# Performance work log

Measured on AMD Instinct MI355X. Metric: run time of the kernel, lower is better.

The kernel has to match this reference:

```python
import jax, jax.numpy as jnp
import numpy as np

D_MODEL = 512
D_STATE = 16
D_CONV = 4
EXPAND = 2
HEADDIM = 64
D_INNER = EXPAND * D_MODEL            # 1024
NHEADS = D_INNER // HEADDIM           # 16
CONV_DIM = D_INNER + 2 * D_STATE      # 1056 (x, B, C channels)
D_IN_PROJ = 2 * D_INNER + 2 * D_STATE + NHEADS  # 2096
EPS = 1e-5
B_SZ, L_SEQ = 8, 4096


def _mamba_param_keys(prefix):
    return [prefix + n for n in
            ('in_proj', 'conv_w', 'conv_b', 'dt_bias', 'A_log', 'D', 'norm_w', 'out_proj')]


def _make_mamba_params(key, prefix):
    ks = jax.random.split(key, 4)
    s = 0.02
    return {
        prefix + 'in_proj': jax.random.normal(ks[0], (D_IN_PROJ, D_MODEL), jnp.float32) * s,
        prefix + 'conv_w': jax.random.normal(ks[1], (CONV_DIM, D_CONV), jnp.float32) * s,
        prefix + 'conv_b': jnp.zeros((CONV_DIM,), jnp.float32),
        prefix + 'dt_bias': jax.random.normal(ks[2], (NHEADS,), jnp.float32) * 0.1,
        prefix + 'A_log': jnp.log(jnp.arange(1, NHEADS + 1, dtype=jnp.float32)),
        prefix + 'D': jnp.ones((NHEADS,), jnp.float32),
        prefix + 'norm_w': jnp.ones((D_INNER,), jnp.float32),
        prefix + 'out_proj': jax.random.normal(ks[3], (D_MODEL, D_INNER), jnp.float32) * s,
    }


def setup_inputs() -> dict:
    key = jax.random.key(0)
    kx, kf, kb, kp = jax.random.split(key, 4)
    inp = {'x': jax.random.normal(kx, (B_SZ, L_SEQ, D_MODEL), jnp.float32)}
    inp.update(_make_mamba_params(kf, 'f_'))
    inp.update(_make_mamba_params(kb, 'b_'))
    kp1, kp2 = jax.random.split(kp)
    inp['proj_w'] = jax.random.normal(kp1, (D_MODEL, 2 * D_MODEL), jnp.float32) * 0.02
    inp['proj_b'] = jnp.zeros((D_MODEL,), jnp.float32)
    inp['ln_w'] = jnp.ones((D_MODEL,), jnp.float32)
    inp['ln_b'] = jnp.zeros((D_MODEL,), jnp.float32)
    return inp


def mamba2(x, in_proj, conv_w, conv_b, dt_bias, A_log, Dp, norm_w, out_proj):
    """Mamba2 block (ngroups=1): in_proj -> causal depthwise conv -> selective scan -> gated RMSNorm -> out_proj."""
    B, L, _ = x.shape
    zxbcdt = x @ in_proj.T                               # [B,L,2096]
    z = zxbcdt[..., :D_INNER]                            # gate
    xBC = zxbcdt[..., D_INNER:D_INNER + CONV_DIM]
    dt = jax.nn.softplus(zxbcdt[..., D_INNER + CONV_DIM:] + dt_bias)  # [B,L,H]
    # causal depthwise conv over (x, B, C) channels + SiLU
    xp = jnp.pad(xBC, ((0, 0), (D_CONV - 1, 0), (0, 0)))
    conv = conv_b + sum(xp[:, k:k + L, :] * conv_w[:, k] for k in range(D_CONV))
    xBC = jax.nn.silu(conv)
    xs = xBC[..., :D_INNER].reshape(B, L, NHEADS, HEADDIM)  # [B,L,H,P]
    Bm = xBC[..., D_INNER:D_INNER + D_STATE]                # [B,L,N]
    Cm = xBC[..., D_INNER + D_STATE:]                       # [B,L,N]
    A = -jnp.exp(A_log)                                     # [H]
    dA = jnp.exp(dt * A)                                    # [B,L,H]

    def step(h, inp):
        dA_t, dt_t, x_t, B_t, C_t = inp                     # [B,H],[B,H],[B,H,P],[B,N],[B,N]
        h = h * dA_t[..., None, None] + (dt_t[..., None] * x_t)[..., None] * B_t[:, None, None, :]
        y = jnp.einsum('bhpn,bn->bhp', h, C_t)
        return h, y

    h0 = jnp.zeros((B, NHEADS, HEADDIM, D_STATE), x.dtype)
    inps = (dA.transpose(1, 0, 2), dt.transpose(1, 0, 2), xs.transpose(1, 0, 2, 3),
            Bm.transpose(1, 0, 2), Cm.transpose(1, 0, 2))
    _, ys = jax.lax.scan(step, h0, inps)                    # ys: [L,B,H,P]
    y = ys.transpose(1, 0, 2, 3) + Dp[:, None] * xs         # skip connection
    y = y.reshape(B, L, D_INNER)
    # gated RMSNorm (norm_before_gate=False)
    y = y * jax.nn.silu(z)
    y = y * jax.lax.rsqrt(jnp.mean(y * y, axis=-1, keepdims=True) + EPS) * norm_w
    return y @ out_proj.T


def _layer_norm(x, w, b):
    mu = jnp.mean(x, axis=-1, keepdims=True)
    v = jnp.var(x, axis=-1, keepdims=True)
    return (x - mu) * jax.lax.rsqrt(v + EPS) * w + b


def reference(x,
              f_in_proj, f_conv_w, f_conv_b, f_dt_bias, f_A_log, f_D, f_norm_w, f_out_proj,
              b_in_proj, b_conv_w, b_conv_b, b_dt_bias, b_A_log, b_D, b_norm_w, b_out_proj,
              proj_w, proj_b, ln_w, ln_b):
    x_fwd = mamba2(x, f_in_proj, f_conv_w, f_conv_b, f_dt_bias, f_A_log, f_D, f_norm_w, f_out_proj)
    x_bwd = jnp.flip(
        mamba2(jnp.flip(x, axis=1), b_in_proj, b_conv_w, b_conv_b, b_dt_bias, b_A_log, b_D, b_norm_w, b_out_proj),
        axis=1)
    comb = jnp.concatenate([x_fwd, x_bwd], axis=-1)         # [B,L,2D]
    out = comb @ proj_w.T + proj_b                          # dropout is identity (eval / p=0)
    return _layer_norm(x + out, ln_w, ln_b)
```

## Files before the change

### kernel.cpp

```cpp
#include <hip/hip_runtime.h>
#include <hip/hip_bf16.h>
#include <math.h>

typedef __bf16 bf16x8_t __attribute__((ext_vector_type(8)));
typedef float f32x4_t __attribute__((ext_vector_type(4)));
typedef unsigned short u16x8_t __attribute__((ext_vector_type(8)));
typedef unsigned short u16x4_t __attribute__((ext_vector_type(4)));

#define DEV __device__ __forceinline__

DEV float bf2f(unsigned short u) {
    unsigned int v = ((unsigned int)u) << 16;
    return __builtin_bit_cast(float, v);
}
DEV unsigned short f2bf(float f) {
    unsigned int u = __builtin_bit_cast(unsigned int, f);
    u += 0x7fffu + ((u >> 16) & 1u);
    return (unsigned short)(u >> 16);
}

__global__ __launch_bounds__(256) void cvt_k(
    const float* __restrict__ in, unsigned short* __restrict__ out, int n8)
{
    int t = blockIdx.x * 256 + threadIdx.x;
    if (t >= n8) return;
    f32x4_t a = ((const f32x4_t*)in)[t * 2];
    f32x4_t b = ((const f32x4_t*)in)[t * 2 + 1];
    u16x8_t o;
#pragma unroll
    for (int j = 0; j < 4; j++) { o[j] = f2bf(a[j]); o[4 + j] = f2bf(b[j]); }
    ((u16x8_t*)out)[t] = o;
}

template <int NT, bool FLIP_A, bool FLIP_C, bool OUT_F32, bool ADD_BIAS, bool ACCUM>
__global__ __launch_bounds__(256, 2) void gemm_bt(
    const unsigned short* __restrict__ A,
    const unsigned short* __restrict__ W,
    void* __restrict__ Cout,
    const float* __restrict__ bias,
    int N, int K, int ldc, int col_ofs)
{
    __shared__ __attribute__((aligned(16))) unsigned char smem[49152];
    const int tid  = threadIdx.x;
    const int wave = tid >> 6;
    const int lane = tid & 63;

    int mtile_i, ntile_i;
    if (NT == 0) {
        mtile_i = blockIdx.y;
        ntile_i = blockIdx.x;
    } else {
        const int L = blockIdx.x;
        const int MTl = (int)gridDim.x / NT;
        const int ppx = MTl >> 3;
        const int xcd = L & 7, q = L >> 3;
        mtile_i = xcd * ppx + q / NT;
        ntile_i = q % NT;
    }
    const int mtile = mtile_i << 7;
    const int ntile = ntile_i << 7;

    const int c0 = tid, c1 = 256 + tid;
    const int r0 = c0 >> 2, p0 = c0 & 3, g0 = p0 ^ ((r0 >> 1) & 3);
    const int r1 = c1 >> 2, p1 = c1 & 3, g1 = p1 ^ ((r1 >> 1) & 3);

    int am0 = mtile + r0; if (FLIP_A) am0 ^= 4095;
    int am1 = mtile + r1; if (FLIP_A) am1 ^= 4095;
    const unsigned short* aP0 = A + (size_t)am0 * K + g0 * 8;
    const unsigned short* aP1 = A + (size_t)am1 * K + g1 * 8;

    int wr0 = ntile + r0; if (wr0 > N - 1) wr0 = N - 1;
    int wr1 = ntile + r1; if (wr1 > N - 1) wr1 = N - 1;
    const unsigned short* wP0 = W + (size_t)wr0 * K + g0 * 8;
    const unsigned short* wP1 = W + (size_t)wr1 * K + g1 * 8;

    const int stago = wave * 1024;

    f32x4_t acc[4][4] = {};

    const int wm = (wave & 1) << 6;
    const int wn = (wave >> 1) << 6;
    const int r    = lane & 15;
    const int quad = lane >> 4;
    const int sw   = (r >> 1) & 3;

    int aoff[4], woff[4];
#pragma unroll
    for (int i = 0; i < 4; i++) {
        int m = wm + i * 16 + r;
        aoff[i] = (m * 4 + (quad ^ sw)) * 16;
        int n = wn + i * 16 + r;
        woff[i] = (n * 4 + (quad ^ sw)) * 16 + 8192;
    }

    auto STAGE = [&](int kt, int bufsel) {
        const int k0 = kt << 5;
        unsigned char* base = smem + bufsel * 16384;
        __builtin_amdgcn_global_load_lds(
            (const __attribute__((address_space(1))) void*)(aP0 + k0),
            (__attribute__((address_space(3))) void*)(base + stago), 16, 0, 0);
        __builtin_amdgcn_global_load_lds(
            (const __attribute__((address_space(1))) void*)(aP1 + k0),
            (__attribute__((address_space(3))) void*)(base + 4096 + stago), 16, 0, 0);
        __builtin_amdgcn_global_load_lds(
            (const __attribute__((address_space(1))) void*)(wP0 + k0),
            (__attribute__((address_space(3))) void*)(base + 8192 + stago), 16, 0, 0);
        __builtin_amdgcn_global_load_lds(
            (const __attribute__((address_space(1))) void*)(wP1 + k0),
            (__attribute__((address_space(3))) void*)(base + 12288 + stago), 16, 0, 0);
    };

    const int nt = K >> 5;
    STAGE(0, 0);
    if (nt > 1) STAGE(1, 1);

    for (int kt = 0; kt < nt; kt++) {
        if (kt + 1 < nt) asm volatile("s_waitcnt vmcnt(4)" ::: "memory");
        else             asm volatile("s_waitcnt vmcnt(0)" ::: "memory");
        __builtin_amdgcn_s_barrier();
        __builtin_amdgcn_sched_barrier(0);

        if (kt + 2 < nt) STAGE(kt + 2, (kt + 2) % 3);

        const unsigned char* bufc = smem + (kt % 3) * 16384;
        bf16x8_t af[4], wf[4];
#pragma unroll
        for (int i = 0; i < 4; i++)
            af[i] = __builtin_bit_cast(bf16x8_t, *(const u16x8_t*)(bufc + aoff[i]));
#pragma unroll
        for (int j = 0; j < 4; j++)
            wf[j] = __builtin_bit_cast(bf16x8_t, *(const u16x8_t*)(bufc + woff[j]));
#pragma unroll
        for (int i = 0; i < 4; i++)
#pragma unroll
            for (int j = 0; j < 4; j++)
                acc[i][j] = __builtin_amdgcn_mfma_f32_16x16x32_bf16(af[i], wf[j], acc[i][j], 0, 0, 0);
        __builtin_amdgcn_sched_barrier(0);
        __builtin_amdgcn_s_barrier();
    }

#pragma unroll
    for (int i = 0; i < 4; i++) {
#pragma unroll
        for (int j = 0; j < 4; j++) {
            int cc = ntile + wn + j * 16 + r;
            if (cc >= N) continue;
#pragma unroll
            for (int reg = 0; reg < 4; reg++) {
                int rr = mtile + wm + i * 16 + quad * 4 + reg;
                int orow = FLIP_C ? (rr ^ 4095) : rr;
                float v = acc[i][j][reg];
                if (ADD_BIAS) v += bias[cc];
                if (OUT_F32) {
                    float* p = (float*)Cout + (size_t)orow * ldc + col_ofs + cc;
                    if (ACCUM) v += *p;
                    *p = v;
                } else {
                    ((unsigned short*)Cout)[(size_t)orow * ldc + col_ofs + cc] = f2bf(v);
                }
            }
        }
    }
}

__global__ __launch_bounds__(256) void pack_pw_k(
    const float* __restrict__ pw, unsigned short* __restrict__ pwb)
{
    int t = blockIdx.x * 256 + threadIdx.x;
    int j8 = t & 63;
    int n  = (t >> 6) & 511;
    int dir = t >> 15;
    const float* src = pw + (size_t)n * 1024 + dir * 512 + j8 * 8;
    f32x4_t a = *(const f32x4_t*)src;
    f32x4_t b = *(const f32x4_t*)(src + 4);
    u16x8_t o;
#pragma unroll
    for (int j = 0; j < 4; j++) { o[j] = f2bf(a[j]); o[4 + j] = f2bf(b[j]); }
    *(u16x8_t*)(pwb + (size_t)dir * 512 * 512 + (size_t)n * 512 + j8 * 8) = o;
}

__global__ __launch_bounds__(256) void tr_op_k(
    const float* __restrict__ op0, const float* __restrict__ op1,
    unsigned short* __restrict__ opT)
{
    __shared__ float tile[32][33];
    const int dir = blockIdx.z;
    const float* op = dir ? op1 : op0;
    const int k0 = blockIdx.x * 32;
    const int j0 = blockIdx.y * 32;
    const int tx = threadIdx.x & 31, ty = threadIdx.x >> 5;
#pragma unroll
    for (int i = 0; i < 4; i++) {
        int j = j0 + ty + i * 8;
        tile[ty + i * 8][tx] = op[(size_t)j * 1024 + k0 + tx];
    }
    __syncthreads();
    unsigned short* dst = opT + (size_t)dir * 1024 * 512;
#pragma unroll
    for (int i = 0; i < 4; i++) {
        int k = k0 + ty + i * 8;
        dst[(size_t)k * 512 + j0 + tx] = f2bf(tile[tx][ty + i * 8]);
    }
}

__global__ __launch_bounds__(256) void conv_silu_k(
    const unsigned short* __restrict__ xin,
    const float* __restrict__ cw,
    const float* __restrict__ cb,
    unsigned short* __restrict__ outp)
{
    int t = blockIdx.x * 256 + threadIdx.x;
    int c8 = t % 132;
    int rb = t / 132;
    int c = c8 * 8;
    int row0 = rb * 8;
    int l0 = row0 & 4095;

    float w[8][4];
#pragma unroll
    for (int j = 0; j < 8; j++) {
        f32x4_t wv = *(const f32x4_t*)(cw + (c + j) * 4);
        w[j][0] = wv[0]; w[j][1] = wv[1]; w[j][2] = wv[2]; w[j][3] = wv[3];
    }
    float bia[8];
    {
        f32x4_t b0 = *(const f32x4_t*)(cb + c);
        f32x4_t b1 = *(const f32x4_t*)(cb + c + 4);
#pragma unroll
        for (int j = 0; j < 4; j++) { bia[j] = b0[j]; bia[4 + j] = b1[j]; }
    }

    u16x8_t zero;
#pragma unroll
    for (int j = 0; j < 8; j++) zero[j] = 0;

    u16x8_t win[11];
#pragma unroll
    for (int u = 0; u < 11; u++) {
        int lu = l0 - 3 + u;
        win[u] = (lu >= 0)
            ? *(const u16x8_t*)(xin + (size_t)(row0 - 3 + u) * 1072 + c)
            : zero;
    }

#pragma unroll
    for (int s = 0; s < 8; s++) {
        float acc[8];
#pragma unroll
        for (int j = 0; j < 8; j++) acc[j] = bia[j];
#pragma unroll
        for (int k = 0; k < 4; k++) {
            u16x8_t xv = win[s + k];
#pragma unroll
            for (int j = 0; j < 8; j++)
                acc[j] = fmaf(bf2f(xv[j]), w[j][k], acc[j]);
        }
        u16x8_t o;
#pragma unroll
        for (int j = 0; j < 8; j++) {
            float xx = acc[j];
            o[j] = f2bf(xx * __builtin_amdgcn_rcpf(1.f + __expf(-xx)));
        }
        *(u16x8_t*)(outp + (size_t)(row0 + s) * 1056 + c) = o;
    }
}

__global__ __launch_bounds__(256) void dt_pre_k(
    const unsigned short* __restrict__ xin,
    const float* __restrict__ dt_bias,
    const float* __restrict__ A_log,
    float* __restrict__ dtb, float* __restrict__ ldab)
{
    int t = blockIdx.x * 256 + threadIdx.x;
    int h = t & 15;
    int row = t >> 4;
    float x = bf2f(xin[(size_t)row * 1072 + 1056 + h]) + dt_bias[h];
    float dt = (x > 20.f) ? x : log1pf(__expf(x));
    float A = -__expf(A_log[h]);
    dtb[t] = dt;
    ldab[t] = dt * A;
}

DEV void stage_xt(const unsigned short* __restrict__ xrow, unsigned short* XtW, int l)
{
    u16x8_t xv[8];
#pragma unroll
    for (int m = 0; m < 8; m++) xv[m] = *(const u16x8_t*)(xrow + m * 8);
#pragma unroll
    for (int p = 0; p < 64; p++) {
        int blkc = (l >> 3) ^ (p & 7);
        XtW[p * 64 + blkc * 8 + (l & 7)] = xv[p >> 3][p & 7];
    }
}

DEV bf16x8_t xt_frag(const unsigned short* XtW, int r, int quad, int jj, int kk)
{
    int p = jj * 16 + r;
    int blkc = (kk * 4 + quad) ^ (p & 7);
    return __builtin_bit_cast(bf16x8_t, *(const u16x8_t*)(XtW + p * 64 + blkc * 8));
}

__global__ __launch_bounds__(256) void scan_chstate_k(
    const unsigned short* __restrict__ xc,
    const float* __restrict__ dtb,
    float* __restrict__ lcs,
    float* __restrict__ Hend, float* __restrict__ dec)
{
    __shared__ __attribute__((aligned(16))) unsigned char sm[37120];
    unsigned short* Btr = (unsigned short*)sm;
    float* csW = (float*)(sm + 2304);
    float* dtW = (float*)(sm + 3328);
    unsigned short* Xt0 = (unsigned short*)(sm + 4352);

    const int tid = threadIdx.x;
    const int w = tid >> 6, l = tid & 63;
    const int r = l & 15, quad = l >> 4;
    const int row0 = blockIdx.x * 64;
    const int b = blockIdx.x >> 6, chunk = blockIdx.x & 63;
    const int h = blockIdx.y * 4 + w;
    const int blk = ((b * 16 + h) << 6) | chunk;

    {
        int n = tid & 15, s0 = (tid >> 4) * 4;
#pragma unroll
        for (int js = 0; js < 4; js++) {
            int s = s0 + js;
            Btr[n * 72 + s] = xc[(size_t)(row0 + s) * 1056 + 1024 + n];
        }
    }

    float v   = lcs[(size_t)(row0 + l) * 16 + h];
    float dtv = dtb[(size_t)(row0 + l) * 16 + h];
#pragma unroll
    for (int d = 1; d < 64; d <<= 1) {
        float o = __shfl_up(v, d, 64);
        if (l >= d) v += o;
    }
    lcs[(size_t)(row0 + l) * 16 + h] = v;
    csW[w * 64 + l] = v;
    dtW[w * 64 + l] = dtv;
    if (l == 63) dec[blk] = __expf(v);
    __syncthreads();

    unsigned short* XtW = Xt0 + w * 4096;
    stage_xt(xc + (size_t)(row0 + l) * 1056 + h * 64, XtW, l);

    const float* csr = csW + w * 64;
    const float* dtr = dtW + w * 64;
    float cs63 = csr[63];

    f32x4_t z = {0.f, 0.f, 0.f, 0.f};
    f32x4_t hacc[4] = {z, z, z, z};
#pragma unroll
    for (int kk = 0; kk < 2; kk++) {
        int sb = kk * 32 + quad * 8;
        u16x8_t bv = *(const u16x8_t*)(Btr + r * 72 + sb);
        f32x4_t c0 = *(const f32x4_t*)(csr + sb);
        f32x4_t c1 = *(const f32x4_t*)(csr + sb + 4);
        f32x4_t d0 = *(const f32x4_t*)(dtr + sb);
        f32x4_t d1 = *(const f32x4_t*)(dtr + sb + 4);
        u16x8_t wv;
#pragma unroll
        for (int j = 0; j < 4; j++) {
            wv[j]     = f2bf(bf2f(bv[j])     * d0[j] * __expf(cs63 - c0[j]));
            wv[4 + j] = f2bf(bf2f(bv[4 + j]) * d1[j] * __expf(cs63 - c1[j]));
        }
        bf16x8_t wf = __builtin_bit_cast(bf16x8_t, wv);
#pragma unroll
        for (int jj = 0; jj < 4; jj++)
            hacc[jj] = __builtin_amdgcn_mfma_f32_16x16x32_bf16(wf, xt_frag(XtW, r, quad, jj, kk), hacc[jj], 0, 0, 0);
    }
    float* o = Hend + (size_t)blk * 1024;
#pragma unroll
    for (int jj = 0; jj < 4; jj++)
#pragma unroll
        for (int reg = 0; reg < 4; reg++)
            o[(jj * 16 + r) * 16 + quad * 4 + reg] = hacc[jj][reg];
}

__global__ __launch_bounds__(64) void scan_comb_k(float* __restrict__ H, const float* __restrict__ dec)
{
    int bh = blockIdx.x >> 2;
    int q  = blockIdx.x & 3;
    int t  = threadIdx.x;
    float* base = H + (size_t)bh * 64 * 1024 + q * 256 + t * 4;
    const float* dp = dec + bh * 64;
    f32x4_t hs = {0.f, 0.f, 0.f, 0.f};
    f32x4_t cur = *(const f32x4_t*)base;
    for (int c = 0; c < 64; c++) {
        int cn = (c < 63) ? c + 1 : 63;
        f32x4_t nxt = *(const f32x4_t*)(base + (size_t)cn * 1024);
        float d = dp[c];
        *(f32x4_t*)(base + (size_t)c * 1024) = hs;
#pragma unroll
        for (int j = 0; j < 4; j++) hs[j] = fmaf(hs[j], d, cur[j]);
        cur = nxt;
    }
}

__global__ __launch_bounds__(256) void scan_chout_k(
    const unsigned short* __restrict__ xc,
    const float* __restrict__ dtb, const float* __restrict__ csb,
    const float* __restrict__ Hst, const float* __restrict__ Dp,
    unsigned short* __restrict__ ybuf)
{
    __shared__ __attribute__((aligned(16))) unsigned char sm[60416];
    unsigned short* Ct = (unsigned short*)sm;
    unsigned short* Bt = (unsigned short*)(sm + 4096);
    float* S   = (float*)(sm + 8192);
    float* csL = (float*)(sm + 25600);
    float* dtL = (float*)(sm + 26624);
    unsigned short* Xt0 = (unsigned short*)(sm + 27648);

    const int tid = threadIdx.x;
    const int w = tid >> 6, l = tid & 63;
    const int r = l & 15, quad = l >> 4;
    const int row0 = blockIdx.x * 64;
    const int b = blockIdx.x >> 6, chunk = blockIdx.x & 63;
    const int h = blockIdx.y * 4 + w;
    const int blk = ((b * 16 + h) << 6) | chunk;

    {
        int rowi = tid >> 2, seg = tid & 3;
        u16x8_t vb, vc;
        if (seg < 2) {
            const unsigned short* src = xc + (size_t)(row0 + rowi) * 1056 + 1024 + seg * 8;
            vb = *(const u16x8_t*)src;
            vc = *(const u16x8_t*)(src + 16);
        } else {
#pragma unroll
            for (int j = 0; j < 8; j++) { vb[j] = 0; vc[j] = 0; }
        }
        *(u16x8_t*)(Bt + rowi * 32 + seg * 8) = vb;
        *(u16x8_t*)(Ct + rowi * 32 + seg * 8) = vc;
    }
    csL[w * 64 + l] = csb[(size_t)(row0 + l) * 16 + h];
    dtL[w * 64 + l] = dtb[(size_t)(row0 + l) * 16 + h];
    __syncthreads();

    {
        bf16x8_t cf = __builtin_bit_cast(bf16x8_t, *(const u16x8_t*)(Ct + (w * 16 + r) * 32 + quad * 8));
        f32x4_t z = {0.f, 0.f, 0.f, 0.f};
#pragma unroll
        for (int j = 0; j < 4; j++) {
            bf16x8_t bfv = __builtin_bit_cast(bf16x8_t, *(const u16x8_t*)(Bt + (j * 16 + r) * 32 + quad * 8));
            f32x4_t d = __builtin_amdgcn_mfma_f32_16x16x32_bf16(cf, bfv, z, 0, 0, 0);
#pragma unroll
            for (int reg = 0; reg < 4; reg++)
                S[(w * 16 + quad * 4 + reg) * 68 + j * 16 + r] = d[reg];
        }
    }
    __syncthreads();

    unsigned short* XtW = Xt0 + w * 4096;
    stage_xt(xc + (size_t)(row0 + l) * 1056 + h * 64, XtW, l);

    const float* csr = csL + w * 64;
    const float* dtr = dtL + w * 64;

    f32x4_t acc[4][4];
    {
        bf16x8_t hf[4];
#pragma unroll
        for (int jj = 0; jj < 4; jj++) {
            int p = jj * 16 + r;
            u16x8_t hv;
            if (quad < 2) {
                const float* hp = Hst + (size_t)blk * 1024 + p * 16 + quad * 8;
                f32x4_t h0 = *(const f32x4_t*)hp;
                f32x4_t h1 = *(const f32x4_t*)(hp + 4);
#pragma unroll
                for (int j = 0; j < 4; j++) { hv[j] = f2bf(h0[j]); hv[4 + j] = f2bf(h1[j]); }
            } else {
#pragma unroll
                for (int j = 0; j < 8; j++) hv[j] = 0;
            }
            hf[jj] = __builtin_bit_cast(bf16x8_t, hv);
        }
        f32x4_t z = {0.f, 0.f, 0.f, 0.f};
#pragma unroll
        for (int i = 0; i < 4; i++) {
            bf16x8_t cf = __builtin_bit_cast(bf16x8_t, *(const u16x8_t*)(Ct + (i * 16 + r) * 32 + quad * 8));
#pragma unroll
            for (int jj = 0; jj < 4; jj++)
                acc[i][jj] = __builtin_amdgcn_mfma_f32_16x16x32_bf16(cf, hf[jj], z, 0, 0, 0);
        }
#pragma unroll
        for (int i = 0; i < 4; i++) {
            f32x4_t es;
#pragma unroll
            for (int reg = 0; reg < 4; reg++) es[reg] = __expf(csr[i * 16 + quad * 4 + reg]);
#pragma unroll
            for (int jj = 0; jj < 4; jj++)
#pragma unroll
                for (int reg = 0; reg < 4; reg++) acc[i][jj][reg] *= es[reg];
        }
    }

#pragma unroll
    for (int kk = 0; kk < 2; kk++) {
        int sb = kk * 32 + quad * 8;
        bf16x8_t xf[4];
#pragma unroll
        for (int jj = 0; jj < 4; jj++) xf[jj] = xt_frag(XtW, r, quad, jj, kk);
        f32x4_t c0 = *(const f32x4_t*)(csr + sb);
        f32x4_t c1 = *(const f32x4_t*)(csr + sb + 4);
        f32x4_t d0 = *(const f32x4_t*)(dtr + sb);
        f32x4_t d1 = *(const f32x4_t*)(dtr + sb + 4);
#pragma unroll
        for (int i = 0; i < 4; i++) {
            int t = i * 16 + r;
            float cst = csr[t];
            const float* Srow = S + t * 68;
            f32x4_t s0 = *(const f32x4_t*)(Srow + sb);
            f32x4_t s1 = *(const f32x4_t*)(Srow + sb + 4);
            u16x8_t wv;
#pragma unroll
            for (int j = 0; j < 4; j++) {
                int s = sb + j;
                float v0 = (s <= t) ? __expf(cst - c0[j]) * d0[j] * s0[j] : 0.f;
                wv[j] = f2bf(v0);
                int s2 = sb + 4 + j;
                float v1 = (s2 <= t) ? __expf(cst - c1[j]) * d1[j] * s1[j] : 0.f;
                wv[4 + j] = f2bf(v1);
            }
            bf16x8_t wf = __builtin_bit_cast(bf16x8_t, wv);
#pragma unroll
            for (int jj = 0; jj < 4; jj++)
                acc[i][jj] = __builtin_amdgcn_mfma_f32_16x16x32_bf16(wf, xf[jj], acc[i][jj], 0, 0, 0);
        }
    }

    float Dh = Dp[h];
#pragma unroll
    for (int i = 0; i < 4; i++) {
#pragma unroll
        for (int jj = 0; jj < 4; jj++) {
            int p = jj * 16 + r;
            int t0 = i * 16 + quad * 4;
            int blk2 = (t0 >> 3) ^ (p & 7);
            u16x4_t x4 = *(const u16x4_t*)(XtW + p * 64 + blk2 * 8 + (t0 & 7));
#pragma unroll
            for (int reg = 0; reg < 4; reg++) {
                float yv = fmaf(Dh, bf2f(x4[reg]), acc[i][jj][reg]);
                ybuf[(size_t)(row0 + t0 + reg) * 1024 + h * 64 + p] = f2bf(yv);
            }
        }
    }
}

__global__ __launch_bounds__(256) void rmsgate_k(
    unsigned short* __restrict__ y,
    const unsigned short* __restrict__ z,
    const float* __restrict__ nw)
{
    const int wave = threadIdx.x >> 6, lane = threadIdx.x & 63;
    const size_t row = (size_t)blockIdx.x * 4 + wave;
    const int c = lane * 16;
    unsigned short* yp = y + row * 1024 + c;
    const unsigned short* zp = z + row * 1024 + c;
    u16x8_t yv0 = *(const u16x8_t*)yp;
    u16x8_t yv1 = *(const u16x8_t*)(yp + 8);
    u16x8_t zv0 = *(const u16x8_t*)zp;
    u16x8_t zv1 = *(const u16x8_t*)(zp + 8);
    float g[16];
    float ss = 0.f;
#pragma unroll
    for (int j = 0; j < 8; j++) {
        float zf = bf2f(zv0[j]);
        float sil = zf * __builtin_amdgcn_rcpf(1.f + __expf(-zf));
        g[j] = bf2f(yv0[j]) * sil;
        ss += g[j] * g[j];
    }
#pragma unroll
    for (int j = 0; j < 8; j++) {
        float zf = bf2f(zv1[j]);
        float sil = zf * __builtin_amdgcn_rcpf(1.f + __expf(-zf));
        g[8 + j] = bf2f(yv1[j]) * sil;
        ss += g[8 + j] * g[8 + j];
    }
#pragma unroll
    for (int m = 32; m > 0; m >>= 1) ss += __shfl_xor(ss, m, 64);
    float scale = rsqrtf(ss * (1.f / 1024.f) + 1e-5f);
    f32x4_t w0 = *(const f32x4_t*)(nw + c);
    f32x4_t w1 = *(const f32x4_t*)(nw + c + 4);
    f32x4_t w2 = *(const f32x4_t*)(nw + c + 8);
    f32x4_t w3 = *(const f32x4_t*)(nw + c + 12);
    u16x8_t o0, o1;
#pragma unroll
    for (int j = 0; j < 4; j++) {
        o0[j]     = f2bf(g[j]      * scale * w0[j]);
        o0[4 + j] = f2bf(g[4 + j]  * scale * w1[j]);
        o1[j]     = f2bf(g[8 + j]  * scale * w2[j]);
        o1[4 + j] = f2bf(g[12 + j] * scale * w3[j]);
    }
    *(u16x8_t*)yp = o0;
    *(u16x8_t*)(yp + 8) = o1;
}

__global__ __launch_bounds__(256) void ln_k(
    const float* __restrict__ x,
    const float* __restrict__ f,
    const float* __restrict__ lw,
    const float* __restrict__ lb,
    float* __restrict__ outp)
{
    const int wave = threadIdx.x >> 6, lane = threadIdx.x & 63;
    const size_t row = (size_t)blockIdx.x * 4 + wave;
    const int c = lane * 8;
    f32x4_t xv0 = *(const f32x4_t*)(x + row * 512 + c);
    f32x4_t xv1 = *(const f32x4_t*)(x + row * 512 + c + 4);
    f32x4_t fv0 = *(const f32x4_t*)(f + row * 512 + c);
    f32x4_t fv1 = *(const f32x4_t*)(f + row * 512 + c + 4);
    float s[8];
    float sum = 0.f, sq = 0.f;
#pragma unroll
    for (int j = 0; j < 4; j++) {
        s[j] = xv0[j] + fv0[j];
        s[4 + j] = xv1[j] + fv1[j];
    }
#pragma unroll
    for (int j = 0; j < 8; j++) { sum += s[j]; sq += s[j] * s[j]; }
#pragma unroll
    for (int m = 32; m > 0; m >>= 1) {
        sum += __shfl_xor(sum, m, 64);
        sq  += __shfl_xor(sq, m, 64);
    }
    float mu = sum * (1.f / 512.f);
    float var = sq * (1.f / 512.f) - mu * mu;
    if (var < 0.f) var = 0.f;
    float inv = rsqrtf(var + 1e-5f);
    f32x4_t w0 = *(const f32x4_t*)(lw + c);
    f32x4_t w1 = *(const f32x4_t*)(lw + c + 4);
    f32x4_t b0 = *(const f32x4_t*)(lb + c);
    f32x4_t b1 = *(const f32x4_t*)(lb + c + 4);
    f32x4_t o0, o1;
#pragma unroll
    for (int j = 0; j < 4; j++) {
        o0[j] = (s[j] - mu) * inv * w0[j] + b0[j];
        o1[j] = (s[4 + j] - mu) * inv * w1[j] + b1[j];
    }
    *(f32x4_t*)(outp + row * 512 + c) = o0;
    *(f32x4_t*)(outp + row * 512 + c + 4) = o1;
}

extern "C" void kernel_launch(void* const* d_in, const int* in_sizes, int n_in,
                              void* d_out, int out_size, void* d_ws, size_t ws_size,
                              hipStream_t stream)
{
    (void)in_sizes; (void)n_in; (void)out_size;

    const float* x           = (const float*)d_in[0];
    const float* in_proj[2]  = {(const float*)d_in[1],  (const float*)d_in[9]};
    const float* conv_w[2]   = {(const float*)d_in[2],  (const float*)d_in[10]};
    const float* conv_b[2]   = {(const float*)d_in[3],  (const float*)d_in[11]};
    const float* dt_bias[2]  = {(const float*)d_in[4],  (const float*)d_in[12]};
    const float* A_log[2]    = {(const float*)d_in[5],  (const float*)d_in[13]};
    const float* Dp[2]       = {(const float*)d_in[6],  (const float*)d_in[14]};
    const float* norm_w[2]   = {(const float*)d_in[7],  (const float*)d_in[15]};
    const float* out_proj[2] = {(const float*)d_in[8],  (const float*)d_in[16]};
    const float* proj_w      = (const float*)d_in[17];
    const float* proj_b      = (const float*)d_in[18];
    const float* ln_w        = (const float*)d_in[19];
    const float* ln_b        = (const float*)d_in[20];
    float* outp = (float*)d_out;

    const size_t IP_ELEMS = (size_t)2096 * 512;
    const size_t X_ELEMS  = (size_t)32768 * 512;

    const size_t constBytes = X_ELEMS * 2 + 2 * IP_ELEMS * 2 + 2 * 512 * 1024 * 2
                            + 2 * 512 * 512 * 2 + 2 * 1024 * 512 * 2 + 8192;
    int g = 1;
    {
        const int cands[3] = {8, 4, 2};
        for (int ci = 0; ci < 3; ci++) {
            size_t R = (size_t)cands[ci] * 4096;
            size_t need = constBytes + R * (2144 + 2112 + 2048 + 64 + 64 + 1024)
                        + (size_t)cands[ci] * 1024 * 4 + 16 * 256;
            if (need <= ws_size) { g = cands[ci]; break; }
        }
    }
    const size_t R = (size_t)g * 4096;
    const int nGroups = 8 / g;
    const int MT = (int)(R >> 7);

    char* ws = (char*)d_ws;
    size_t off = 0;
    auto alloc = [&](size_t bytes) -> char* {
        char* p = ws + off;
        off += (bytes + 255) & ~(size_t)255;
        return p;
    };
    unsigned short* xb16  = (unsigned short*)alloc(X_ELEMS * 2);
    unsigned short* ipb16[2];
    ipb16[0] = (unsigned short*)alloc(IP_ELEMS * 2);
    ipb16[1] = (unsigned short*)alloc(IP_ELEMS * 2);
    unsigned short* Ebuf  = (unsigned short*)alloc(2 * 512 * 1024 * 2);
    unsigned short* Ef    = Ebuf;
    unsigned short* Eb    = Ebuf + 512 * 1024;
    unsigned short* pwb   = (unsigned short*)alloc(2 * 512 * 512 * 2);
    unsigned short* opT   = (unsigned short*)alloc(2 * 1024 * 512 * 2);
    unsigned short* xbcdt = (unsigned short*)alloc(R * 1072 * 2);
    unsigned short* ybuf  = xbcdt;
    unsigned short* xconv = (unsigned short*)alloc(R * 1056 * 2);
    unsigned short* zbuf  = xconv;
    float* fbuf = (float*)alloc(R * 512 * 4);
    float* dtb  = (float*)alloc(R * 16 * 4);
    float* dab  = (float*)alloc(R * 16 * 4);
    float* Hbuf = (float*)alloc(R * 1024);
    float* dec  = (float*)alloc((size_t)g * 1024 * 4);

    dim3 blk(256);

    cvt_k<<<(unsigned)((X_ELEMS / 8 + 255) / 256), blk, 0, stream>>>(x, xb16, (int)(X_ELEMS / 8));
    cvt_k<<<(unsigned)((IP_ELEMS / 8 + 255) / 256), blk, 0, stream>>>(in_proj[0], ipb16[0], (int)(IP_ELEMS / 8));
    cvt_k<<<(unsigned)((IP_ELEMS / 8 + 255) / 256), blk, 0, stream>>>(in_proj[1], ipb16[1], (int)(IP_ELEMS / 8));
    pack_pw_k<<<256, blk, 0, stream>>>(proj_w, pwb);
    tr_op_k<<<dim3(32, 16, 2), blk, 0, stream>>>(out_proj[0], out_proj[1], opT);
    gemm_bt<0, false, false, false, false, false><<<dim3(8, 4), blk, 0, stream>>>(
        pwb, opT, Ef, nullptr, 1024, 512, 1024, 0);
    gemm_bt<0, false, false, false, false, false><<<dim3(8, 4), blk, 0, stream>>>(
        pwb + 512 * 512, opT + 1024 * 512, Eb, nullptr, 1024, 512, 1024, 0);

    for (int grp = 0; grp < nGroups; grp++) {
        const unsigned short* xg = xb16 + (size_t)grp * R * 512;
        const float* xgf = x + (size_t)grp * R * 512;
        float* og = outp + (size_t)grp * R * 512;

        for (int dir = 0; dir < 2; dir++) {
            if (dir == 0)
                gemm_bt<9, false, false, false, false, false><<<(unsigned)(9 * MT), blk, 0, stream>>>(
                    xg, ipb16[0] + (size_t)1024 * 512, xbcdt, nullptr, 1072, 512, 1072, 0);
            else
                gemm_bt<9, true, false, false, false, false><<<(unsigned)(9 * MT), blk, 0, stream>>>(
                    xg, ipb16[1] + (size_t)1024 * 512, xbcdt, nullptr, 1072, 512, 1072, 0);

            conv_silu_k<<<(unsigned)(R * 132 / 2048), blk, 0, stream>>>(xbcdt, conv_w[dir], conv_b[dir], xconv);
            dt_pre_k<<<(unsigned)(R * 16 / 256), blk, 0, stream>>>(xbcdt, dt_bias[dir], A_log[dir], dtb, dab);

            scan_chstate_k<<<dim3((unsigned)(R / 64), 4), blk, 0, stream>>>(xconv, dtb, dab, Hbuf, dec);
            scan_comb_k<<<(unsigned)(g * 64), dim3(64), 0, stream>>>(Hbuf, dec);
            scan_chout_k<<<dim3((unsigned)(R / 64), 4), blk, 0, stream>>>(xconv, dtb, dab, Hbuf, Dp[dir], ybuf);

            if (dir == 0)
                gemm_bt<8, false, false, false, false, false><<<(unsigned)(8 * MT), blk, 0, stream>>>(
                    xg, ipb16[0], zbuf, nullptr, 1024, 512, 1024, 0);
            else
                gemm_bt<8, true, false, false, false, false><<<(unsigned)(8 * MT), blk, 0, stream>>>(
                    xg, ipb16[1], zbuf, nullptr, 1024, 512, 1024, 0);

            rmsgate_k<<<(unsigned)(R / 4), blk, 0, stream>>>(ybuf, zbuf, norm_w[dir]);

            if (dir == 0)
                gemm_bt<4, false, false, true, true, false><<<(unsigned)(4 * MT), blk, 0, stream>>>(
                    ybuf, Ef, fbuf, proj_b, 512, 1024, 512, 0);
            else
                gemm_bt<4, false, true, true, false, true><<<(unsigned)(4 * MT), blk, 0, stream>>>(
                    ybuf, Eb, fbuf, nullptr, 512, 1024, 512, 0);
        }
        ln_k<<<(unsigned)(R / 4), blk, 0, stream>>>(xgf, fbuf, ln_w, ln_b, og);
    }
}
```

Before: 885.3 us.

## Enlarge GEMM block tile to 256x128 with 8 waves sharing W tile

The bf16 MFMA GEMM moves from 256 threads on a 128x128 tile to 512 threads on a 256x128 tile. Each weight tile staged in LDS is now reused by twice as many rows, which cuts global weight traffic and per-tile overhead. LDS grows to 72KB per block across three stages, so occupancy may drop and the grid shrinks to half as many blocks. The epilogue code is not shown, so it is unclear whether it was updated for the new wave-to-row mapping.

New measurement: 897.9 us. No clear change (+1.4%).

```diff
diff --git a/kernel.cpp b/kernel.cpp
--- a/kernel.cpp
+++ b/kernel.cpp
@@ -33,14 +33,14 @@
 }
 
 template <int NT, bool FLIP_A, bool FLIP_C, bool OUT_F32, bool ADD_BIAS, bool ACCUM>
-__global__ __launch_bounds__(256, 2) void gemm_bt(
+__global__ __launch_bounds__(512, 2) void gemm_bt(
     const unsigned short* __restrict__ A,
     const unsigned short* __restrict__ W,
     void* __restrict__ Cout,
     const float* __restrict__ bias,
     int N, int K, int ldc, int col_ofs)
 {
-    __shared__ __attribute__((aligned(16))) unsigned char smem[49152];
+    __shared__ __attribute__((aligned(16))) unsigned char smem[73728];
     const int tid  = threadIdx.x;
     const int wave = tid >> 6;
     const int lane = tid & 63;
@@ -57,29 +57,28 @@
         mtile_i = xcd * ppx + q / NT;
         ntile_i = q % NT;
     }
-    const int mtile = mtile_i << 7;
+    const int mtile = mtile_i << 8;
     const int ntile = ntile_i << 7;
 
-    const int c0 = tid, c1 = 256 + tid;
-    const int r0 = c0 >> 2, p0 = c0 & 3, g0 = p0 ^ ((r0 >> 1) & 3);
-    const int r1 = c1 >> 2, p1 = c1 & 3, g1 = p1 ^ ((r1 >> 1) & 3);
-
-    int am0 = mtile + r0; if (FLIP_A) am0 ^= 4095;
-    int am1 = mtile + r1; if (FLIP_A) am1 ^= 4095;
-    const unsigned short* aP0 = A + (size_t)am0 * K + g0 * 8;
-    const unsigned short* aP1 = A + (size_t)am1 * K + g1 * 8;
-
-    int wr0 = ntile + r0; if (wr0 > N - 1) wr0 = N - 1;
-    int wr1 = ntile + r1; if (wr1 > N - 1) wr1 = N - 1;
-    const unsigned short* wP0 = W + (size_t)wr0 * K + g0 * 8;
-    const unsigned short* wP1 = W + (size_t)wr1 * K + g1 * 8;
+    const int cA0 = tid, cA1 = 512 + tid;
+    const int rA0 = cA0 >> 2, pA0 = cA0 & 3, gA0 = pA0 ^ ((rA0 >> 1) & 3);
+    const int rA1 = cA1 >> 2, pA1 = cA1 & 3, gA1 = pA1 ^ ((rA1 >> 1) & 3);
+    const int rW  = tid >> 2, pW  = tid & 3, gW  = pW  ^ ((rW  >> 1) & 3);
+
+    int am0 = mtile + rA0; if (FLIP_A) am0 ^= 4095;
+    int am1 = mtile + rA1; if (FLIP_A) am1 ^= 4095;
+    const unsigned short* aP0 = A + (size_t)am0 * K + gA0 * 8;
+    const unsigned short* aP1 = A + (size_t)am1 * K + gA1 * 8;
+
+    int wr = ntile + rW; if (wr > N - 1) wr = N - 1;
+    const unsigned short* wP = W + (size_t)wr * K + gW * 8;
 
     const int stago = wave * 1024;
 
     f32x4_t acc[4][4] = {};
 
-    const int wm = (wave & 1) << 6;
-    const int wn = (wave >> 1) << 6;
+    const int wm = ((wave >> 1) & 3) << 6;
+    const int wn = (wave & 1) << 6;
     const int r    = lane & 15;
     const int quad = lane >> 4;
     const int sw   = (r >> 1) & 3;
@@ -90,24 +89,21 @@
         int m = wm + i * 16 + r;
         aoff[i] = (m * 4 + (quad ^ sw)) * 16;
         int n = wn + i * 16 + r;
-        woff[i] = (n * 4 + (quad ^ sw)) * 16 + 8192;
+        woff[i] = 16384 + (n * 4 + (quad ^ sw)) * 16;
     }
 
     auto STAGE = [&](int kt, int bufsel) {
         const int k0 = kt << 5;
-        unsigned char* base = smem + bufsel * 16384;
+        unsigned char* base = smem + bufsel * 24576;
         __builtin_amdgcn_global_load_lds(
             (const __attribute__((address_space(1))) void*)(aP0 + k0),
             (__attribute__((address_space(3))) void*)(base + stago), 16, 0, 0);
         __builtin_amdgcn_global_load_lds(
             (const __attribute__((address_space(1))) void*)(aP1 + k0),
-            (__attribute__((address_space(3))) void*)(base + 4096 + stago), 16, 0, 0);
-        __builtin_amdgcn_global_load_lds(
-            (const __attribute__((address_space(1))) void*)(wP0 + k0),
             (__attribute__((address_space(3))) void*)(base + 8192 + stago), 16, 0, 0);
         __builtin_amdgcn_global_load_lds(
-            (const __attribute__((address_space(1))) void*)(wP1 + k0),
-            (__attribute__((address_space(3))) void*)(base + 12288 + stago), 16, 0, 0);
+            (const __attribute__((address_space(1))) void*)(wP + k0),
+            (__attribute__((address_space(3))) void*)(base + 16384 + stago), 16, 0, 0);
     };
 
     const int nt = K >> 5;
@@ -115,14 +111,14 @@
     if (nt > 1) STAGE(1, 1);
 
     for (int kt = 0; kt < nt; kt++) {
-        if (kt + 1 < nt) asm volatile("s_waitcnt vmcnt(4)" ::: "memory");
+        if (kt + 1 < nt) asm volatile("s_waitcnt vmcnt(3)" ::: "memory");
         else             asm volatile("s_waitcnt vmcnt(0)" ::: "memory");
         __builtin_amdgcn_s_barrier();
         __builtin_amdgcn_sched_barrier(0);
 
         if (kt + 2 < nt) STAGE(kt + 2, (kt + 2) % 3);
 
-        const unsigned char* bufc = smem + (kt % 3) * 16384;
+        const unsigned char* bufc = smem + (kt % 3) * 24576;
         bf16x8_t af[4], wf[4];
 #pragma unroll
         for (int i = 0; i < 4; i++)
@@ -682,7 +678,7 @@
     }
     const size_t R = (size_t)g * 4096;
     const int nGroups = 8 / g;
-    const int MT = (int)(R >> 7);
+    const int MT2 = (int)(R >> 8);
 
     char* ws = (char*)d_ws;
     size_t off = 0;
@@ -711,15 +707,16 @@
     float* dec  = (float*)alloc((size_t)g * 1024 * 4);
 
     dim3 blk(256);
+    dim3 blkg(512);
 
     cvt_k<<<(unsigned)((X_ELEMS / 8 + 255) / 256), blk, 0, stream>>>(x, xb16, (int)(X_ELEMS / 8));
     cvt_k<<<(unsigned)((IP_ELEMS / 8 + 255) / 256), blk, 0, stream>>>(in_proj[0], ipb16[0], (int)(IP_ELEMS / 8));
     cvt_k<<<(unsigned)((IP_ELEMS / 8 + 255) / 256), blk, 0, stream>>>(in_proj[1], ipb16[1], (int)(IP_ELEMS / 8));
     pack_pw_k<<<256, blk, 0, stream>>>(proj_w, pwb);
     tr_op_k<<<dim3(32, 16, 2), blk, 0, stream>>>(out_proj[0], out_proj[1], opT);
-    gemm_bt<0, false, false, false, false, false><<<dim3(8, 4), blk, 0, stream>>>(
+    gemm_bt<0, false, false, false, false, false><<<dim3(8, 2), blkg, 0, stream>>>(
         pwb, opT, Ef, nullptr, 1024, 512, 1024, 0);
-    gemm_bt<0, false, false, false, false, false><<<dim3(8, 4), blk, 0, stream>>>(
+    gemm_bt<0, false, false, false, false, false><<<dim3(8, 2), blkg, 0, stream>>>(
         pwb + 512 * 512, opT + 1024 * 512, Eb, nullptr, 1024, 512, 1024, 0);
 
     for (int grp = 0; grp < nGroups; grp++) {
@@ -729,10 +726,10 @@
 
         for (int dir = 0; dir < 2; dir++) {
             if (dir == 0)
-                gemm_bt<9, false, false, false, false, false><<<(unsigned)(9 * MT), blk, 0, stream>>>(
+                gemm_bt<9, false, false, false, false, false><<<(unsigned)(9 * MT2), blkg, 0, stream>>>(
                     xg, ipb16[0] + (size_t)1024 * 512, xbcdt, nullptr, 1072, 512, 1072, 0);
             else
-                gemm_bt<9, true, false, false, false, false><<<(unsigned)(9 * MT), blk, 0, stream>>>(
+                gemm_bt<9, true, false, false, false, false><<<(unsigned)(9 * MT2), blkg, 0, stream>>>(
                     xg, ipb16[1] + (size_t)1024 * 512, xbcdt, nullptr, 1072, 512, 1072, 0);
 
             conv_silu_k<<<(unsigned)(R * 132 / 2048), blk, 0, stream>>>(xbcdt, conv_w[dir], conv_b[dir], xconv);
@@ -743,19 +740,19 @@
             scan_chout_k<<<dim3((unsigned)(R / 64), 4), blk, 0, stream>>>(xconv, dtb, dab, Hbuf, Dp[dir], ybuf);
 
             if (dir == 0)
-                gemm_bt<8, false, false, false, false, false><<<(unsigned)(8 * MT), blk, 0, stream>>>(
+                gemm_bt<8, false, false, false, false, false><<<(unsigned)(8 * MT2), blkg, 0, stream>>>(
                     xg, ipb16[0], zbuf, nullptr, 1024, 512, 1024, 0);
             else
-                gemm_bt<8, true, false, false, false, false><<<(unsigned)(8 * MT), blk, 0, stream>>>(
+                gemm_bt<8, true, false, false, false, false><<<(unsigned)(8 * MT2), blkg, 0, stream>>>(
                     xg, ipb16[1], zbuf, nullptr, 1024, 512, 1024, 0);
 
             rmsgate_k<<<(unsigned)(R / 4), blk, 0, stream>>>(ybuf, zbuf, norm_w[dir]);
 
             if (dir == 0)
-                gemm_bt<4, false, false, true, true, false><<<(unsigned)(4 * MT), blk, 0, stream>>>(
+                gemm_bt<4, false, false, true, true, false><<<(unsigned)(4 * MT2), blkg, 0, stream>>>(
                     ybuf, Ef, fbuf, proj_b, 512, 1024, 512, 0);
             else
-                gemm_bt<4, false, true, true, false, true><<<(unsigned)(4 * MT), blk, 0, stream>>>(
+                gemm_bt<4, false, true, true, false, true><<<(unsigned)(4 * MT2), blkg, 0, stream>>>(
                     ybuf, Eb, fbuf, nullptr, 512, 1024, 512, 0);
         }
         ln_k<<<(unsigned)(R / 4), blk, 0, stream>>>(xgf, fbuf, ln_w, ln_b, og);
```
